# Performance work log

Measured on AMD Instinct MI355X. Metric: run time of the kernel, lower is better.

Reference implementation:

```python
import jax, jax.numpy as jnp
import numpy as np

V, E, H = 50000, 200, 256
B, R, S, W = 16, 16, 16, 32


def gru_last(x, Wih, Whh, bih, bhh):
    """PyTorch-style GRU, return final hidden state.
    x: [N, T, D]; Wih: [3H, D]; Whh: [3H, H]. Gate order: r, z, n."""
    gx = jnp.einsum('ntd,gd->ntg', x, Wih) + bih  # precompute input gates [N,T,3H]
    h0 = jnp.zeros((x.shape[0], Whh.shape[1]), x.dtype)

    def step(h, gxt):
        gh = h @ Whh.T + bhh
        xr, xz, xn = jnp.split(gxt, 3, axis=-1)
        hr, hz, hn = jnp.split(gh, 3, axis=-1)
        r = jax.nn.sigmoid(xr + hr)
        z = jax.nn.sigmoid(xz + hz)
        n = jnp.tanh(xn + r * hn)
        return (1.0 - z) * n + z * h, None

    h, _ = jax.lax.scan(step, h0, jnp.swapaxes(gx, 0, 1))
    return h  # [N, H]


def mlp(x, W1, b1, W2, b2):
    # Linear -> SELU -> (Dropout is identity in eval) -> Linear
    return jax.nn.selu(x @ W1.T + b1) @ W2.T + b2


def setup_inputs() -> dict:
    key = jax.random.key(0)
    ks = jax.random.split(key, 20)
    n = lambda k, shp: (jax.random.normal(k, shp, dtype=jnp.float32) * 0.05)
    inp = {
        'inputs': jax.random.randint(ks[0], (B, R, S, W), 0, V, dtype=jnp.int64),
        'emb': n(ks[1], (V, E)),
        'w_Wih': n(ks[2], (3 * H, E)), 'w_Whh': n(ks[3], (3 * H, H)),
        'w_bih': n(ks[4], (3 * H,)), 'w_bhh': n(ks[5], (3 * H,)),
        's_Wih': n(ks[6], (3 * H, H)), 's_Whh': n(ks[7], (3 * H, H)),
        's_bih': n(ks[8], (3 * H,)), 's_bhh': n(ks[9], (3 * H,)),
        'r_Wih': n(ks[10], (3 * H, H)), 'r_Whh': n(ks[11], (3 * H, H)),
        'r_bih': n(ks[12], (3 * H,)), 'r_bhh': n(ks[13], (3 * H,)),
        'rfc_W1': n(ks[14], (H // 2, H)), 'rfc_b1': n(ks[15], (H // 2,)),
        'rfc_W2': n(ks[16], (1, H // 2)), 'rfc_b2': jnp.zeros((1,), jnp.float32),
        'pfc_W1': n(ks[17], (H // 2, H)), 'pfc_b1': n(ks[18], (H // 2,)),
        'pfc_W2': n(ks[19], (1, H // 2)), 'pfc_b2': jnp.zeros((1,), jnp.float32),
    }
    return inp


def reference(inputs, emb, w_Wih, w_Whh, w_bih, w_bhh,
              s_Wih, s_Whh, s_bih, s_bhh,
              r_Wih, r_Whh, r_bih, r_bhh,
              rfc_W1, rfc_b1, rfc_W2, rfc_b2,
              pfc_W1, pfc_b1, pfc_W2, pfc_b2):
    b, r, s, w = inputs.shape
    x = emb[inputs]                                   # [B,R,S,W,E] (dropout = identity in eval)
    # word-level GRU over all sentences at once (batches the Python double loop)
    sent_h = gru_last(x.reshape(b * r * s, w, E), w_Wih, w_Whh, w_bih, w_bhh)  # [B*R*S, H]
    # sentence-level GRU per review
    rev_h = gru_last(sent_h.reshape(b * r, s, H), s_Wih, s_Whh, s_bih, s_bhh)  # [B*R, H]
    p_batch = rev_h.reshape(b, r, H)                  # [B, R, H]
    r_stars = mlp(p_batch, rfc_W1, rfc_b1, rfc_W2, rfc_b2)  # [B, R, 1]
    # review-level GRU per business
    biz_h = gru_last(p_batch, r_Wih, r_Whh, r_bih, r_bhh)   # [B, H]
    b_stars = mlp(biz_h, pfc_W1, pfc_b1, pfc_W2, pfc_b2)    # [B, 1]
    return (b_stars, r_stars)
```

## Files before the change

### kernel.cpp

```cpp
#include <hip/hip_runtime.h>
#include <math.h>

#define VOCAB 50000
#define EDIM  200
#define HDIM  256
#define G3    768
#define NSEQ1 4096
#define T1    32
#define NSEQ2 256
#define T2    16
#define NSEQ3 16
#define T3    16

using bf16x8 = __attribute__((ext_vector_type(8))) short;
using f32x4  = __attribute__((ext_vector_type(4))) float;

__device__ __forceinline__ float sigmoid_f(float x) {
    return 1.0f / (1.0f + __expf(-x));
}
__device__ __forceinline__ float tanh_f(float x) {
    return 1.0f - 2.0f / (__expf(2.0f * x) + 1.0f);
}
__device__ __forceinline__ short f2b(float f) {
    unsigned u = __float_as_uint(f);
    unsigned r = (u + 0x7fffu + ((u >> 16) & 1u)) >> 16;
    return (short)r;
}
__device__ __forceinline__ float b2f(unsigned short v) {
    return __uint_as_float((unsigned)v << 16);
}
__device__ __forceinline__ void lds_barrier() {
    asm volatile("s_waitcnt lgkmcnt(0)\n\ts_barrier" ::: "memory");
}

struct CvtJob { const float* src; short* dst; int kin; int kpad; };
struct CvtJobs { CvtJob j[6]; };

__global__ void convert6(CvtJobs jobs) {
    const CvtJob jb = jobs.j[blockIdx.y];
    const int r = blockIdx.x;
    for (int k = threadIdx.x; k < jb.kpad; k += blockDim.x)
        jb.dst[(size_t)r * jb.kpad + k] =
            (k < jb.kin) ? f2b(jb.src[(size_t)r * jb.kin + k]) : (short)0;
}

template <int KC, bool AF32>
__global__ __launch_bounds__(512) void gemm_mfma(
    const void* __restrict__ Av, const short* __restrict__ WB,
    const float* __restrict__ bias, unsigned* __restrict__ Cv,
    int M, int Keff) {
    constexpr int KPAD  = KC * 32;
    constexpr int CELLS = KPAD / 8;
    __shared__ short As[128 * 256];
    const int tid = threadIdx.x;
    const int m0 = blockIdx.x * 128;
    const int n0 = blockIdx.y * 192;

    {
        const int row  = tid >> 2;
        const int c0   = (tid & 3) * 8;
        const int rowg = m0 + row;
        const int vcell = Keff >> 3;
        for (int i = 0; i < 8; i++) {
            const int c = c0 + i;
            if (c >= CELLS) break;
            bf16x8 v;
            if (rowg < M && c < vcell) {
                if constexpr (AF32) {
                    const float* ap = (const float*)Av + (size_t)rowg * Keff + c * 8;
                    const float4 x = *(const float4*)ap;
                    const float4 y = *(const float4*)(ap + 4);
                    v[0] = f2b(x.x); v[1] = f2b(x.y); v[2] = f2b(x.z); v[3] = f2b(x.w);
                    v[4] = f2b(y.x); v[5] = f2b(y.y); v[6] = f2b(y.z); v[7] = f2b(y.w);
                } else {
                    const short* ap = (const short*)Av + (size_t)rowg * Keff + c * 8;
                    v = *(const bf16x8*)ap;
                }
            } else {
                v = (bf16x8)(short)0;
            }
            *(bf16x8*)&As[row * 256 + ((c ^ (row & 7)) << 3)] = v;
        }
    }
    __syncthreads();

    const int w  = tid >> 6;
    const int l  = tid & 63;
    const int lr = l & 15, lg = l >> 4;

    bf16x8 af[KC];
    {
        const int row = (w << 4) + lr;
#pragma unroll
        for (int kc = 0; kc < KC; kc++) {
            const int cell = kc * 4 + lg;
            af[kc] = *(const bf16x8*)&As[row * 256 + ((cell ^ (row & 7)) << 3)];
        }
    }
    f32x4 acc[12];
#pragma unroll
    for (int nt = 0; nt < 12; nt++) acc[nt] = (f32x4){0.f, 0.f, 0.f, 0.f};
#pragma unroll
    for (int nt = 0; nt < 12; nt++) {
        const short* wb = WB + (size_t)(n0 + nt * 16 + lr) * KPAD + lg * 8;
#pragma unroll
        for (int kc = 0; kc < KC; kc++) {
            bf16x8 bf = *(const bf16x8*)(wb + kc * 32);
            acc[nt] = __builtin_amdgcn_mfma_f32_16x16x32_bf16(af[kc], bf, acc[nt], 0, 0, 0);
        }
    }
    const int by12 = blockIdx.y * 12;
#pragma unroll
    for (int nt = 0; nt < 12; nt += 2) {
        const int gt = by12 + nt;
        const int g  = gt >> 4;
        const int pp = (gt & 15) >> 1;
        const int uoff = pp * 48 + lr * 3 + g;
        const float bv0 = bias[n0 + nt * 16 + lr];
        const float bv1 = bias[n0 + (nt + 1) * 16 + lr];
#pragma unroll
        for (int q = 0; q < 4; q++) {
            const int row = m0 + (w << 4) + lg * 4 + q;
            if (row < M) {
                const unsigned lo = (unsigned short)f2b(acc[nt][q] + bv0);
                const unsigned hi = (unsigned short)f2b(acc[nt + 1][q] + bv1);
                Cv[(size_t)row * 384 + uoff] = lo | (hi << 16);
            }
        }
    }
}

__global__ __launch_bounds__(512, 2) void gru_mfma(
    const int* __restrict__ idx,
    const short* __restrict__ gxb,
    const short* __restrict__ WB,
    const float* __restrict__ bhh,
    short* __restrict__ hb16,
    const float* __restrict__ mW1,
    const float* __restrict__ mb1,
    const float* __restrict__ mW2,
    const float* __restrict__ mb2,
    float* __restrict__ mOut,
    int T) {
    __shared__ __align__(16) short wsN[256 * 256];
    __shared__ __align__(16) short hs0[16 * 256];
    __shared__ __align__(16) short hs1[16 * 256];
    __shared__ int idxs[16 * T1];
    const int tid = threadIdx.x;
    const int n0 = blockIdx.x * 16;
    const int w  = tid >> 6, l = tid & 63;
    const int lr = l & 15, lg = l >> 4;
    const int jj0 = w * 32 + lr;
    const int jj1 = jj0 + 16;

    for (int i = tid; i < 16 * 256; i += 512) hs0[i] = 0;
    if (idx) {
        for (int i = tid; i < 16 * T; i += 512) {
            const int s = i / T, p = i - s * T;
            int tk = idx[(size_t)(n0 + s) * T + p];
            idxs[s * T + p] = min(max(tk, 0), VOCAB - 1);
        }
    }
#pragma unroll
    for (int i = 0; i < 16; i++) {
        const int cellidx = tid * 16 + i;
        const int rr = cellidx >> 5;
        const int cc = cellidx & 31;
        bf16x8 v = *(const bf16x8*)&WB[(size_t)(512 + rr) * 256 + cc * 8];
        *(bf16x8*)&wsN[rr * 256 + ((cc ^ (rr & 7)) << 3)] = v;
    }
    bf16x8 bwR[2][8], bwZ[2][8];
#pragma unroll
    for (int ti = 0; ti < 2; ti++) {
        const int jjt = (w * 2 + ti) * 16 + lr;
#pragma unroll
        for (int kc = 0; kc < 8; kc++) {
            bwR[ti][kc] = *(const bf16x8*)&WB[(size_t)jjt * 256 + kc * 32 + lg * 8];
            bwZ[ti][kc] = *(const bf16x8*)&WB[(size_t)(256 + jjt) * 256 + kc * 32 + lg * 8];
        }
    }
    const float bR0 = bhh[jj0],       bR1 = bhh[jj1];
    const float bZ0 = bhh[256 + jj0], bZ1 = bhh[256 + jj1];
    const float bN0 = bhh[512 + jj0], bN1 = bhh[512 + jj1];

    float hreg[2][4] = {};
    __syncthreads();

    uint3 gA[4], gB[4];
    auto load_gx = [&](uint3 (&buf)[4], int t) {
#pragma unroll
        for (int q = 0; q < 4; q++) {
            const int s = lg * 4 + q;
            size_t rowbase;
            if (idx) rowbase = (size_t)idxs[s * T + t] * G3;
            else     rowbase = ((size_t)(n0 + s) * T + t) * G3;
            buf[q] = *(const uint3*)(gxb + rowbase + w * 96 + lr * 6);
        }
    };

    auto step = [&](const uint3 (&buf)[4], const short* hsR, short* hsW) {
        f32x4 aR[2], aZ[2], aN[2];
#pragma unroll
        for (int ti = 0; ti < 2; ti++) {
            aR[ti] = (f32x4){0.f, 0.f, 0.f, 0.f};
            aZ[ti] = (f32x4){0.f, 0.f, 0.f, 0.f};
            aN[ti] = (f32x4){0.f, 0.f, 0.f, 0.f};
        }
#pragma unroll
        for (int kc = 0; kc < 8; kc++) {
            const int cell = kc * 4 + lg;
            const bf16x8 a   = *(const bf16x8*)&hsR[lr * 256 + ((cell ^ (lr & 7)) << 3)];
            const bf16x8 n0f = *(const bf16x8*)&wsN[jj0 * 256 + ((cell ^ (jj0 & 7)) << 3)];
            const bf16x8 n1f = *(const bf16x8*)&wsN[jj1 * 256 + ((cell ^ (jj1 & 7)) << 3)];
            aR[0] = __builtin_amdgcn_mfma_f32_16x16x32_bf16(a, bwR[0][kc], aR[0], 0, 0, 0);
            aZ[0] = __builtin_amdgcn_mfma_f32_16x16x32_bf16(a, bwZ[0][kc], aZ[0], 0, 0, 0);
            aN[0] = __builtin_amdgcn_mfma_f32_16x16x32_bf16(a, n0f, aN[0], 0, 0, 0);
            aR[1] = __builtin_amdgcn_mfma_f32_16x16x32_bf16(a, bwR[1][kc], aR[1], 0, 0, 0);
            aZ[1] = __builtin_amdgcn_mfma_f32_16x16x32_bf16(a, bwZ[1][kc], aZ[1], 0, 0, 0);
            aN[1] = __builtin_amdgcn_mfma_f32_16x16x32_bf16(a, n1f, aN[1], 0, 0, 0);
        }
#pragma unroll
        for (int q = 0; q < 4; q++) {
            const int s = lg * 4 + q;
            const uint3 u = buf[q];
            {
                const float xr = b2f((unsigned short)(u.x & 0xffff));
                const float xz = b2f((unsigned short)(u.y & 0xffff));
                const float xn = b2f((unsigned short)(u.z & 0xffff));
                const float r = sigmoid_f(xr + aR[0][q] + bR0);
                const float z = sigmoid_f(xz + aZ[0][q] + bZ0);
                const float n = tanh_f(xn + r * (aN[0][q] + bN0));
                const float h = (1.f - z) * n + z * hreg[0][q];
                hreg[0][q] = h;
                hsW[s * 256 + (((jj0 >> 3) ^ (s & 7)) << 3) + (jj0 & 7)] = f2b(h);
            }
            {
                const float xr = b2f((unsigned short)(u.x >> 16));
                const float xz = b2f((unsigned short)(u.y >> 16));
                const float xn = b2f((unsigned short)(u.z >> 16));
                const float r = sigmoid_f(xr + aR[1][q] + bR1);
                const float z = sigmoid_f(xz + aZ[1][q] + bZ1);
                const float n = tanh_f(xn + r * (aN[1][q] + bN1));
                const float h = (1.f - z) * n + z * hreg[1][q];
                hreg[1][q] = h;
                hsW[s * 256 + (((jj1 >> 3) ^ (s & 7)) << 3) + (jj1 & 7)] = f2b(h);
            }
        }
        lds_barrier();
    };

    load_gx(gA, 0);
    for (int t = 0; t < T; t += 2) {
        if (t + 1 < T) load_gx(gB, t + 1);
        step(gA, hs0, hs1);
        if (t + 2 < T) load_gx(gA, t + 2);
        step(gB, hs1, hs0);
    }

    if (hb16) {
#pragma unroll
        for (int q = 0; q < 4; q++) {
            const int s = lg * 4 + q;
            hb16[(size_t)(n0 + s) * HDIM + jj0] = f2b(hreg[0][q]);
            hb16[(size_t)(n0 + s) * HDIM + jj1] = f2b(hreg[1][q]);
        }
    }
    if (mW1) {
        float* hf = (float*)wsN;
#pragma unroll
        for (int q = 0; q < 4; q++) {
            const int s = lg * 4 + q;
            hf[s * HDIM + jj0] = hreg[0][q];
            hf[s * HDIM + jj1] = hreg[1][q];
        }
        lds_barrier();
        const int mm = tid & 127;
        const int sg = tid >> 7;
        const float* w1 = mW1 + (size_t)mm * HDIM;
        const float b1v = mb1[mm];
        const float w2v = mW2[mm];
        float* redf = (float*)hs0;
#pragma unroll
        for (int si = 0; si < 4; si++) {
            const int s = si * 4 + sg;
            const float* hrow = hf + s * HDIM;
            float d = 0.f;
#pragma unroll 4
            for (int k = 0; k < HDIM; k += 4) {
                const float4 a = *(const float4*)&hrow[k];
                const float4 b = *(const float4*)&w1[k];
                d += a.x * b.x; d += a.y * b.y; d += a.z * b.z; d += a.w * b.w;
            }
            d += b1v;
            const float alpha = 1.6732632423543772f;
            const float scale = 1.0507009873554805f;
            const float sv = scale * (d > 0.f ? d : alpha * expm1f(d));
            redf[s * 128 + mm] = sv * w2v;
        }
        lds_barrier();
        if (tid < 16) {
            float accv = mb2[0];
            for (int m = 0; m < 128; m++) accv += redf[tid * 128 + m];
            mOut[n0 + tid] = accv;
        }
    }
}

extern "C" void kernel_launch(void* const* d_in, const int* in_sizes, int n_in,
                              void* d_out, int out_size, void* d_ws, size_t ws_size,
                              hipStream_t stream) {
    const int*   idx    = (const int*)d_in[0];
    const float* emb    = (const float*)d_in[1];
    const float* w_Wih  = (const float*)d_in[2];
    const float* w_Whh  = (const float*)d_in[3];
    const float* w_bih  = (const float*)d_in[4];
    const float* w_bhh  = (const float*)d_in[5];
    const float* s_Wih  = (const float*)d_in[6];
    const float* s_Whh  = (const float*)d_in[7];
    const float* s_bih  = (const float*)d_in[8];
    const float* s_bhh  = (const float*)d_in[9];
    const float* r_Wih  = (const float*)d_in[10];
    const float* r_Whh  = (const float*)d_in[11];
    const float* r_bih  = (const float*)d_in[12];
    const float* r_bhh  = (const float*)d_in[13];
    const float* rfc_W1 = (const float*)d_in[14];
    const float* rfc_b1 = (const float*)d_in[15];
    const float* rfc_W2 = (const float*)d_in[16];
    const float* rfc_b2 = (const float*)d_in[17];
    const float* pfc_W1 = (const float*)d_in[18];
    const float* pfc_b1 = (const float*)d_in[19];
    const float* pfc_W2 = (const float*)d_in[20];
    const float* pfc_b2 = (const float*)d_in[21];

    float* out = (float*)d_out;

    short* sws = (short*)d_ws;
    short* Pb      = sws;
    short* gx2b    = Pb      + (size_t)VOCAB * G3;
    short* gx3b    = gx2b    + (size_t)NSEQ1 * G3;
    short* WhhB_w  = gx3b    + (size_t)NSEQ2 * G3;
    short* WihB_w  = WhhB_w  + (size_t)G3 * HDIM;
    short* sWihB   = WihB_w  + (size_t)G3 * 224;
    short* sWhhB   = sWihB   + (size_t)G3 * HDIM;
    short* rWihB   = sWhhB   + (size_t)G3 * HDIM;
    short* rWhhB   = rWihB   + (size_t)G3 * HDIM;
    short* sent_hB = rWhhB   + (size_t)G3 * HDIM;
    short* rev_hB  = sent_hB + (size_t)NSEQ1 * HDIM;

    CvtJobs jobs;
    jobs.j[0] = {w_Whh, WhhB_w, HDIM, HDIM};
    jobs.j[1] = {w_Wih, WihB_w, EDIM, 224};
    jobs.j[2] = {s_Wih, sWihB, HDIM, HDIM};
    jobs.j[3] = {s_Whh, sWhhB, HDIM, HDIM};
    jobs.j[4] = {r_Wih, rWihB, HDIM, HDIM};
    jobs.j[5] = {r_Whh, rWhhB, HDIM, HDIM};
    convert6<<<dim3(G3, 6), 256, 0, stream>>>(jobs);

    gemm_mfma<7, true><<<dim3((VOCAB + 127) / 128, 4), 512, 0, stream>>>(
        emb, WihB_w, w_bih, (unsigned*)Pb, VOCAB, EDIM);

    gru_mfma<<<NSEQ1 / 16, 512, 0, stream>>>(
        idx, Pb, WhhB_w, w_bhh, sent_hB,
        nullptr, nullptr, nullptr, nullptr, nullptr, T1);

    gemm_mfma<8, false><<<dim3(NSEQ1 / 128, 4), 512, 0, stream>>>(
        sent_hB, sWihB, s_bih, (unsigned*)gx2b, NSEQ1, HDIM);

    gru_mfma<<<NSEQ2 / 16, 512, 0, stream>>>(
        nullptr, gx2b, sWhhB, s_bhh, rev_hB,
        rfc_W1, rfc_b1, rfc_W2, rfc_b2, out + 16, T2);

    gemm_mfma<8, false><<<dim3(2, 4), 512, 0, stream>>>(
        rev_hB, rWihB, r_bih, (unsigned*)gx3b, NSEQ2, HDIM);

    gru_mfma<<<1, 512, 0, stream>>>(
        nullptr, gx3b, rWhhB, r_bhh, nullptr,
        pfc_W1, pfc_b1, pfc_W2, pfc_b2, out, T3);
}
```

Baseline: 728.5 us.

## Split GRU hidden tiles across 16 waves with 1024-thread blocks

The recurrent GRU kernel now runs 1024 threads per block, so each wave owns one 16-column hidden tile instead of two. The per-step MFMA chain per wave is halved and register-resident R/Z weights shrink, aiming for lower step latency on the serial recurrence. The MLP head's final 128-element reduction is also changed from a serial loop over 16 threads to a wave shuffle reduction. In exchange, the launch bound of (1024,4) constrains registers, and each wave loads gx words and discards half.

```diff
diff --git a/kernel.cpp b/kernel.cpp
--- a/kernel.cpp
+++ b/kernel.cpp
@@ -130,7 +130,7 @@
     }
 }
 
-__global__ __launch_bounds__(512, 2) void gru_mfma(
+__global__ __launch_bounds__(1024, 4) void gru_mfma(
     const int* __restrict__ idx,
     const short* __restrict__ gxb,
     const short* __restrict__ WB,
@@ -150,40 +150,36 @@
     const int n0 = blockIdx.x * 16;
     const int w  = tid >> 6, l = tid & 63;
     const int lr = l & 15, lg = l >> 4;
-    const int jj0 = w * 32 + lr;
-    const int jj1 = jj0 + 16;
-
-    for (int i = tid; i < 16 * 256; i += 512) hs0[i] = 0;
+    const int pp = w >> 1, hh = w & 1;
+    const int jj = pp * 32 + hh * 16 + lr;
+
+    for (int i = tid; i < 16 * 256; i += 1024) hs0[i] = 0;
     if (idx) {
-        for (int i = tid; i < 16 * T; i += 512) {
+        for (int i = tid; i < 16 * T; i += 1024) {
             const int s = i / T, p = i - s * T;
             int tk = idx[(size_t)(n0 + s) * T + p];
             idxs[s * T + p] = min(max(tk, 0), VOCAB - 1);
         }
     }
 #pragma unroll
-    for (int i = 0; i < 16; i++) {
-        const int cellidx = tid * 16 + i;
+    for (int i = 0; i < 8; i++) {
+        const int cellidx = tid * 8 + i;
         const int rr = cellidx >> 5;
         const int cc = cellidx & 31;
         bf16x8 v = *(const bf16x8*)&WB[(size_t)(512 + rr) * 256 + cc * 8];
         *(bf16x8*)&wsN[rr * 256 + ((cc ^ (rr & 7)) << 3)] = v;
     }
-    bf16x8 bwR[2][8], bwZ[2][8];
-#pragma unroll
-    for (int ti = 0; ti < 2; ti++) {
-        const int jjt = (w * 2 + ti) * 16 + lr;
-#pragma unroll
-        for (int kc = 0; kc < 8; kc++) {
-            bwR[ti][kc] = *(const bf16x8*)&WB[(size_t)jjt * 256 + kc * 32 + lg * 8];
-            bwZ[ti][kc] = *(const bf16x8*)&WB[(size_t)(256 + jjt) * 256 + kc * 32 + lg * 8];
-        }
-    }
-    const float bR0 = bhh[jj0],       bR1 = bhh[jj1];
-    const float bZ0 = bhh[256 + jj0], bZ1 = bhh[256 + jj1];
-    const float bN0 = bhh[512 + jj0], bN1 = bhh[512 + jj1];
-
-    float hreg[2][4] = {};
+    bf16x8 bwR[8], bwZ[8];
+#pragma unroll
+    for (int kc = 0; kc < 8; kc++) {
+        bwR[kc] = *(const bf16x8*)&WB[(size_t)jj * 256 + kc * 32 + lg * 8];
+        bwZ[kc] = *(const bf16x8*)&WB[(size_t)(256 + jj) * 256 + kc * 32 + lg * 8];
+    }
+    const float bR = bhh[jj];
+    const float bZ = bhh[256 + jj];
+    const float bN = bhh[512 + jj];
+
+    float hreg[4] = {0.f, 0.f, 0.f, 0.f};
     __syncthreads();
 
     uint3 gA[4], gB[4];
@@ -194,57 +190,39 @@
             size_t rowbase;
             if (idx) rowbase = (size_t)idxs[s * T + t] * G3;
             else     rowbase = ((size_t)(n0 + s) * T + t) * G3;
-            buf[q] = *(const uint3*)(gxb + rowbase + w * 96 + lr * 6);
+            buf[q] = *(const uint3*)(gxb + rowbase + pp * 96 + lr * 6);
         }
     };
 
     auto step = [&](const uint3 (&buf)[4], const short* hsR, short* hsW) {
-        f32x4 aR[2], aZ[2], aN[2];
-#pragma unroll
-        for (int ti = 0; ti < 2; ti++) {
-            aR[ti] = (f32x4){0.f, 0.f, 0.f, 0.f};
-            aZ[ti] = (f32x4){0.f, 0.f, 0.f, 0.f};
-            aN[ti] = (f32x4){0.f, 0.f, 0.f, 0.f};
-        }
+        f32x4 aR = (f32x4){0.f, 0.f, 0.f, 0.f};
+        f32x4 aZ = (f32x4){0.f, 0.f, 0.f, 0.f};
+        f32x4 aN = (f32x4){0.f, 0.f, 0.f, 0.f};
 #pragma unroll
         for (int kc = 0; kc < 8; kc++) {
             const int cell = kc * 4 + lg;
-            const bf16x8 a   = *(const bf16x8*)&hsR[lr * 256 + ((cell ^ (lr & 7)) << 3)];
-            const bf16x8 n0f = *(const bf16x8*)&wsN[jj0 * 256 + ((cell ^ (jj0 & 7)) << 3)];
-            const bf16x8 n1f = *(const bf16x8*)&wsN[jj1 * 256 + ((cell ^ (jj1 & 7)) << 3)];
-            aR[0] = __builtin_amdgcn_mfma_f32_16x16x32_bf16(a, bwR[0][kc], aR[0], 0, 0, 0);
-            aZ[0] = __builtin_amdgcn_mfma_f32_16x16x32_bf16(a, bwZ[0][kc], aZ[0], 0, 0, 0);
-            aN[0] = __builtin_amdgcn_mfma_f32_16x16x32_bf16(a, n0f, aN[0], 0, 0, 0);
-            aR[1] = __builtin_amdgcn_mfma_f32_16x16x32_bf16(a, bwR[1][kc], aR[1], 0, 0, 0);
-            aZ[1] = __builtin_amdgcn_mfma_f32_16x16x32_bf16(a, bwZ[1][kc], aZ[1], 0, 0, 0);
-            aN[1] = __builtin_amdgcn_mfma_f32_16x16x32_bf16(a, n1f, aN[1], 0, 0, 0);
+            const bf16x8 a  = *(const bf16x8*)&hsR[lr * 256 + ((cell ^ (lr & 7)) << 3)];
+            const bf16x8 nf = *(const bf16x8*)&wsN[jj * 256 + ((cell ^ (jj & 7)) << 3)];
+            aR = __builtin_amdgcn_mfma_f32_16x16x32_bf16(a, bwR[kc], aR, 0, 0, 0);
+            aZ = __builtin_amdgcn_mfma_f32_16x16x32_bf16(a, bwZ[kc], aZ, 0, 0, 0);
+            aN = __builtin_amdgcn_mfma_f32_16x16x32_bf16(a, nf, aN, 0, 0, 0);
         }
 #pragma unroll
         for (int q = 0; q < 4; q++) {
             const int s = lg * 4 + q;
             const uint3 u = buf[q];
-            {
-                const float xr = b2f((unsigned short)(u.x & 0xffff));
-                const float xz = b2f((unsigned short)(u.y & 0xffff));
-                const float xn = b2f((unsigned short)(u.z & 0xffff));
-                const float r = sigmoid_f(xr + aR[0][q] + bR0);
-                const float z = sigmoid_f(xz + aZ[0][q] + bZ0);
-                const float n = tanh_f(xn + r * (aN[0][q] + bN0));
-                const float h = (1.f - z) * n + z * hreg[0][q];
-                hreg[0][q] = h;
-                hsW[s * 256 + (((jj0 >> 3) ^ (s & 7)) << 3) + (jj0 & 7)] = f2b(h);
-            }
-            {
-                const float xr = b2f((unsigned short)(u.x >> 16));
-                const float xz = b2f((unsigned short)(u.y >> 16));
-                const float xn = b2f((unsigned short)(u.z >> 16));
-                const float r = sigmoid_f(xr + aR[1][q] + bR1);
-                const float z = sigmoid_f(xz + aZ[1][q] + bZ1);
-                const float n = tanh_f(xn + r * (aN[1][q] + bN1));
-                const float h = (1.f - z) * n + z * hreg[1][q];
-                hreg[1][q] = h;
-                hsW[s * 256 + (((jj1 >> 3) ^ (s & 7)) << 3) + (jj1 & 7)] = f2b(h);
-            }
+            const float xr = hh ? b2f((unsigned short)(u.x >> 16))
+                                : b2f((unsigned short)(u.x & 0xffff));
+            const float xz = hh ? b2f((unsigned short)(u.y >> 16))
+                                : b2f((unsigned short)(u.y & 0xffff));
+            const float xn = hh ? b2f((unsigned short)(u.z >> 16))
+                                : b2f((unsigned short)(u.z & 0xffff));
+            const float r = sigmoid_f(xr + aR[q] + bR);
+            const float z = sigmoid_f(xz + aZ[q] + bZ);
+            const float n = tanh_f(xn + r * (aN[q] + bN));
+            const float h = (1.f - z) * n + z * hreg[q];
+            hreg[q] = h;
+            hsW[s * 256 + (((jj >> 3) ^ (s & 7)) << 3) + (jj & 7)] = f2b(h);
         }
         lds_barrier();
     };
@@ -261,8 +239,7 @@
 #pragma unroll
         for (int q = 0; q < 4; q++) {
             const int s = lg * 4 + q;
-            hb16[(size_t)(n0 + s) * HDIM + jj0] = f2b(hreg[0][q]);
-            hb16[(size_t)(n0 + s) * HDIM + jj1] = f2b(hreg[1][q]);
+            hb16[(size_t)(n0 + s) * HDIM + jj] = f2b(hreg[q]);
         }
     }
     if (mW1) {
@@ -270,8 +247,7 @@
 #pragma unroll
         for (int q = 0; q < 4; q++) {
             const int s = lg * 4 + q;
-            hf[s * HDIM + jj0] = hreg[0][q];
-            hf[s * HDIM + jj1] = hreg[1][q];
+            hf[s * HDIM + jj] = hreg[q];
         }
         lds_barrier();
         const int mm = tid & 127;
@@ -281,8 +257,8 @@
         const float w2v = mW2[mm];
         float* redf = (float*)hs0;
 #pragma unroll
-        for (int si = 0; si < 4; si++) {
-            const int s = si * 4 + sg;
+        for (int si = 0; si < 2; si++) {
+            const int s = si * 8 + sg;
             const float* hrow = hf + s * HDIM;
             float d = 0.f;
 #pragma unroll 4
@@ -298,10 +274,11 @@
             redf[s * 128 + mm] = sv * w2v;
         }
         lds_barrier();
-        if (tid < 16) {
-            float accv = mb2[0];
-            for (int m = 0; m < 128; m++) accv += redf[tid * 128 + m];
-            mOut[n0 + tid] = accv;
+        {
+            float v = redf[w * 128 + l] + redf[w * 128 + 64 + l];
+#pragma unroll
+            for (int off = 32; off; off >>= 1) v += __shfl_down(v, off);
+            if (l == 0) mOut[n0 + w] = v + mb2[0];
         }
     }
 }
@@ -359,21 +336,21 @@
     gemm_mfma<7, true><<<dim3((VOCAB + 127) / 128, 4), 512, 0, stream>>>(
         emb, WihB_w, w_bih, (unsigned*)Pb, VOCAB, EDIM);
 
-    gru_mfma<<<NSEQ1 / 16, 512, 0, stream>>>(
+    gru_mfma<<<NSEQ1 / 16, 1024, 0, stream>>>(
         idx, Pb, WhhB_w, w_bhh, sent_hB,
         nullptr, nullptr, nullptr, nullptr, nullptr, T1);
 
     gemm_mfma<8, false><<<dim3(NSEQ1 / 128, 4), 512, 0, stream>>>(
         sent_hB, sWihB, s_bih, (unsigned*)gx2b, NSEQ1, HDIM);
 
-    gru_mfma<<<NSEQ2 / 16, 512, 0, stream>>>(
+    gru_mfma<<<NSEQ2 / 16, 1024, 0, stream>>>(
         nullptr, gx2b, sWhhB, s_bhh, rev_hB,
         rfc_W1, rfc_b1, rfc_W2, rfc_b2, out + 16, T2);
 
     gemm_mfma<8, false><<<dim3(2, 4), 512, 0, stream>>>(
         rev_hB, rWihB, r_bih, (unsigned*)gx3b, NSEQ2, HDIM);
 
-    gru_mfma<<<1, 512, 0, stream>>>(
+    gru_mfma<<<1, 1024, 0, stream>>>(
         nullptr, gx3b, rWhhB, r_bhh, nullptr,
         pfc_W1, pfc_b1, pfc_W2, pfc_b2, out, T3);
 }
```

New measurement: 893.7 us. 22.7% more time.
